# Optimization experiments

Hardware: AMD Instinct MI355X
Metric: run time of the kernel (lower is better)

## Reference

```python
import jax, jax.numpy as jnp
import numpy as np

# lct_fk config (matches init_kwargs)
BIN_LEN = 0.01
WALL_SIZE = 2.0
C_LIGHT = 3.0e8


def _safe_sqrt(v):
    # sqrt(relu(v)) with a well-defined (zero) subgradient at v<=0
    pos = v > 0
    return jnp.where(pos, jnp.sqrt(jnp.where(pos, v, 1.0)), 0.0)


def _trilinear_zero(vol, pz, py, px):
    # vol: (D,H,W) complex64; pz/py/px: (D2,H2,W2) float pixel coords
    # Trilinear sampling with zeros padding (== F.grid_sample align_corners=False)
    D, H, W = vol.shape
    z0f = jnp.floor(pz); y0f = jnp.floor(py); x0f = jnp.floor(px)
    dz = pz - z0f; dy = py - y0f; dx = px - x0f
    z0 = z0f.astype(jnp.int32); y0 = y0f.astype(jnp.int32); x0 = x0f.astype(jnp.int32)
    out = jnp.zeros(pz.shape, vol.dtype)
    for iz, wz in ((z0, 1.0 - dz), (z0 + 1, dz)):
        for iy, wy in ((y0, 1.0 - dy), (y0 + 1, dy)):
            for ix, wx in ((x0, 1.0 - dx), (x0 + 1, dx)):
                valid = (iz >= 0) & (iz < D) & (iy >= 0) & (iy < H) & (ix >= 0) & (ix < W)
                v = vol[jnp.clip(iz, 0, D - 1), jnp.clip(iy, 0, H - 1), jnp.clip(ix, 0, W - 1)]
                w = jnp.where(valid, wz * wy * wx, 0.0)
                out = out + w * v
    return out


def setup_inputs() -> dict:
    key = jax.random.key(0)
    feture = jax.random.uniform(key, (1, 2, 128, 128, 128), dtype=jnp.float32)
    return {"feture_bxdxtxhxw": feture}


def reference(feture_bxdxtxhxw):
    b, d, T, H, W = feture_bxdxtxhxw.shape
    M, N = T, H  # temprol_grid (== crop), sptial_grid; tbes=0, tens=crop -> no temporal pad
    width = WALL_SIZE / 2.0
    trange = M * BIN_LEN  # crop * c * (bin_len/c)

    # z-weighting: (z/(M-1))^2, then sqrt(relu(.))
    gridz = (jnp.arange(M, dtype=jnp.float32) / (M - 1)).reshape(1, M, 1, 1)
    data = feture_bxdxtxhxw.reshape(b * d, T, H, W) * (gridz ** 2)
    data = _safe_sqrt(jax.nn.relu(data))

    # zero-pad to (2T,2H,2W), FFT, fftshift (roll by half == fftshift for even sizes)
    datapad = jnp.pad(data, ((0, 0), (0, M), (0, N), (0, N)))
    fre = jnp.fft.fftshift(jnp.fft.fftn(datapad, axes=(-3, -2, -1)), axes=(-3, -2, -1))

    # Stolt (f-k) warped coordinates, normalized to [-1,1]
    zdim = (jnp.arange(2 * M, dtype=jnp.float32) - M) / M
    xdim = (jnp.arange(2 * N, dtype=jnp.float32) - N) / N
    gz = zdim[:, None, None]            # varies along axis 0
    gy = xdim[None, :, None]            # varies along axis 1
    gx = xdim[None, None, :]            # varies along axis 2
    fk = (N * trange / (M * width * 4.0)) ** 2
    gznew = jnp.sqrt(fk * (gx ** 2 + gy ** 2) + gz ** 2)  # (2M,2N,2N)
    gznew = jnp.broadcast_to(gznew, (2 * M, 2 * N, 2 * N))

    # unnormalize (align_corners=False): pix = ((c+1)*size - 1)/2
    px = ((jnp.broadcast_to(gx, gznew.shape) + 1.0) * (2 * N) - 1.0) * 0.5
    py = ((jnp.broadcast_to(gy, gznew.shape) + 1.0) * (2 * N) - 1.0) * 0.5
    pz = ((gznew + 1.0) * (2 * M) - 1.0) * 0.5

    samp = jax.vmap(lambda v: _trilinear_zero(v, pz, py, px))(fre)

    # zero negative/zero frequencies along z, then Stolt Jacobian scaling
    z0pos = M + 1  # first index where zdim > 0
    zmask = (jnp.arange(2 * M) >= z0pos)[None, :, None, None]
    samp = samp * zmask
    samp = samp * (jnp.abs(gz) / (gznew + 1e-8))[None]

    samp = jnp.fft.fftshift(samp, axes=(-3, -2, -1))  # ifftshift == fftshift (even dims)
    vol = jnp.fft.ifftn(samp, axes=(-3, -2, -1))
    out = vol[:, :M, :N, :N].real
    return out.reshape(b, d, M, N, N)
```

## Files before the change

### kernel.cpp

```cpp
#include <hip/hip_runtime.h>

static constexpr size_t VS   = 8388608;
static constexpr int    ZSTR = 65536;
static constexpr int    YSTR = 256;
static constexpr size_t VSB  = 4194304;
static constexpr int    BZS  = 32768;
static constexpr int    BYS  = 128;
static constexpr int    LSTR = 261;

typedef float vf2 __attribute__((ext_vector_type(2)));
typedef _Float16 h2 __attribute__((ext_vector_type(2)));

__device__ __forceinline__ unsigned pkh(vf2 a){
    h2 h; h.x = (_Float16)a.x; h.y = (_Float16)a.y;
    return __builtin_bit_cast(unsigned, h);
}
__device__ __forceinline__ vf2 uph(unsigned u){
    h2 h = __builtin_bit_cast(h2, u);
    vf2 r; r.x = (float)h.x; r.y = (float)h.y; return r;
}

__device__ __forceinline__ vf2 cmul(vf2 a, vf2 b){
    vf2 asw; asw.x = -a.y; asw.y = a.x;
    return a*b.x + asw*b.y;
}

constexpr int BREV(int k){ return ((k&1)<<3)|((k&2)<<1)|((k&4)>>1)|((k&8)>>3); }

__device__ __forceinline__ void bf(vf2& a, vf2& b, float c, float s){
    vf2 sum = a + b;
    vf2 dif = a - b;
    vf2 dsw; dsw.x = -dif.y; dsw.y = dif.x;
    b = dif*c + dsw*s;
    a = sum;
}

template<int DIR>
__device__ __forceinline__ void fft16(vf2 r[16]){
    constexpr float D = (float)DIR;
    constexpr float C16[8] = {1.f, 0.92387953f, 0.70710678f, 0.38268343f, 0.f, -0.38268343f, -0.70710678f, -0.92387953f};
    constexpr float S16[8] = {0.f, 0.38268343f, 0.70710678f, 0.92387953f, 1.f, 0.92387953f, 0.70710678f, 0.38268343f};
#pragma unroll
    for (int j = 0; j < 8; ++j) bf(r[j], r[j+8], C16[j], D*S16[j]);
    constexpr float C8[4] = {1.f, 0.70710678f, 0.f, -0.70710678f};
    constexpr float S8[4] = {0.f, 0.70710678f, 1.f, 0.70710678f};
#pragma unroll
    for (int g = 0; g < 16; g += 8)
#pragma unroll
        for (int j = 0; j < 4; ++j) bf(r[g+j], r[g+j+4], C8[j], D*S8[j]);
#pragma unroll
    for (int g = 0; g < 16; g += 4){
        bf(r[g],   r[g+2], 1.f, 0.f);
        bf(r[g+1], r[g+3], 0.f, D);
    }
#pragma unroll
    for (int g = 0; g < 16; g += 2) bf(r[g], r[g+1], 1.f, 0.f);
}

__device__ __forceinline__ void init_tw(vf2* tw, float dir){
    int tid = threadIdx.x;
    float ang = dir * 0.0245436926f * (float)((tid >> 4)*(tid & 15));
    float s, c; __sincosf(ang, &s, &c);
    vf2 w; w.x = c; w.y = s;
    tw[tid] = w;
}

template<int DIR>
__device__ __forceinline__ void mid256t2(vf2 r[2][16], unsigned* shp, const vf2* tw, int t, int l){
#pragma unroll
    for (int c = 0; c < 2; ++c) fft16<DIR>(r[c]);
#pragma unroll
    for (int k1 = 1; k1 < 16; ++k1){
        vf2 w = tw[k1*16 + t];
        r[0][BREV(k1)] = cmul(r[0][BREV(k1)], w);
        r[1][BREV(k1)] = cmul(r[1][BREV(k1)], w);
    }
    int lr = l & 7;
    bool lo = (l < 8);
    if (lo){
#pragma unroll
        for (int c = 0; c < 2; ++c)
#pragma unroll
            for (int k1 = 0; k1 < 16; ++k1)
                shp[(lr*2 + c)*LSTR + k1*16 + (t ^ k1)] = pkh(r[c][BREV(k1)]);
    }
    __syncthreads();
    if (lo){
#pragma unroll
        for (int c = 0; c < 2; ++c)
#pragma unroll
            for (int n2 = 0; n2 < 16; ++n2)
                r[c][n2] = uph(shp[(lr*2 + c)*LSTR + t*16 + (n2 ^ t)]);
    }
    __syncthreads();
    if (!lo){
#pragma unroll
        for (int c = 0; c < 2; ++c)
#pragma unroll
            for (int k1 = 0; k1 < 16; ++k1)
                shp[(lr*2 + c)*LSTR + k1*16 + (t ^ k1)] = pkh(r[c][BREV(k1)]);
    }
    __syncthreads();
    if (!lo){
#pragma unroll
        for (int c = 0; c < 2; ++c)
#pragma unroll
            for (int n2 = 0; n2 < 16; ++n2)
                r[c][n2] = uph(shp[(lr*2 + c)*LSTR + t*16 + (n2 ^ t)]);
    }
#pragma unroll
    for (int c = 0; c < 2; ++c) fft16<DIR>(r[c]);
}

template<int DIR>
__device__ __forceinline__ void twiddle_reg(vf2 r[16], int t){
    float sn, cn; __sincosf((float)DIR * 0.0245436926f * (float)t, &sn, &cn);
    vf2 w; w.x = cn; w.y = sn;
    vf2 wk = w;
#pragma unroll
    for (int k1 = 1; k1 < 16; ++k1){
        r[BREV(k1)] = cmul(r[BREV(k1)], wk);
        wk = cmul(wk, w);
    }
}

__device__ __forceinline__ void wave_transpose(vf2 r[16], vf2* shw, int t, int l){
    vf2* base = shw + ((l >> 2)*2 + (l & 1))*LSTR;
    if ((l & 2) == 0){
#pragma unroll
        for (int k1 = 0; k1 < 16; ++k1) base[k1*16 + (t ^ k1)] = r[BREV(k1)];
#pragma unroll
        for (int n2 = 0; n2 < 16; ++n2) r[n2] = base[t*16 + (n2 ^ t)];
    }
    __builtin_amdgcn_sched_barrier(0);
    if ((l & 2) != 0){
#pragma unroll
        for (int k1 = 15; k1 >= 0; --k1) base[k1*16 + (t ^ k1)] = r[BREV(k1)];
#pragma unroll
        for (int n2 = 15; n2 >= 0; --n2) r[n2] = base[t*16 + (n2 ^ t)];
    }
}

template<int DIR>
__device__ __forceinline__ void mid256wr(vf2 r[16], vf2* shw, int t, int l){
    fft16<DIR>(r);
    twiddle_reg<DIR>(r, t);
    wave_transpose(r, shw, t, l);
    fft16<DIR>(r);
}

template<int DIR, int NIN, int NOUT>
__device__ __forceinline__ void fft_strided2(unsigned* g, int S, float insc){
    __shared__ unsigned shp[16*LSTR];
    __shared__ vf2 tw[256];
    int t = threadIdx.x >> 4, l = threadIdx.x & 15;
    vf2 r[2][16];
    vf2 zero; zero.x = 0.f; zero.y = 0.f;
#pragma unroll
    for (int n1 = 0; n1 < 16; ++n1){
        if (n1 < NIN/16){
            uint2 ld = *reinterpret_cast<const uint2*>(&g[(size_t)(16*n1 + t)*S + 2*l]);
            r[0][n1] = uph(ld.x)*insc;
            r[1][n1] = uph(ld.y)*insc;
        } else { r[0][n1] = zero; r[1][n1] = zero; }
    }
    init_tw(tw, (float)DIR);
    __syncthreads();
    mid256t2<DIR>(r, shp, tw, t, l);
#pragma unroll
    for (int k2 = 0; k2 < 16; ++k2)
        if (k2 < NOUT/16){
            uint2 st; st.x = pkh(r[0][BREV(k2)]); st.y = pkh(r[1][BREV(k2)]);
            *reinterpret_cast<uint2*>(&g[(size_t)(t + 16*k2)*S + 2*l]) = st;
        }
}

__global__ void __launch_bounds__(256) k_p1(const float* __restrict__ in, unsigned* __restrict__ A){
    __shared__ vf2 sh8[8*LSTR];
    int tid = threadIdx.x, bid = blockIdx.x;
    int yc = bid & 7, z = (bid >> 3) & 127, v = bid >> 10;
    int t = tid & 15, l = tid >> 4;
    float gz = z * (1.0f/127.0f);
    float g2 = gz*gz;
    const float* src = in + (((size_t)(v*128 + z))*128 + yc*16 + l)*128;
    float val[8];
#pragma unroll
    for (int n1 = 0; n1 < 8; ++n1) val[n1] = src[16*n1 + t];
#pragma unroll
    for (int n1 = 0; n1 < 8; ++n1){
        float x = val[n1] * g2;
        val[n1] = x > 0.f ? sqrtf(x) : 0.f;
    }
    float part = ((val[0]+val[1]) + (val[2]+val[3])) + ((val[4]+val[5]) + (val[6]+val[7]));
    part = (t & 1) ? -part : part;
    part += __shfl_xor(part, 1);
    part += __shfl_xor(part, 2);
    part += __shfl_xor(part, 4);
    part += __shfl_xor(part, 8);
    vf2 r[16];
    vf2 zero; zero.x = 0.f; zero.y = 0.f;
#pragma unroll
    for (int n1 = 8; n1 < 16; ++n1) r[n1] = zero;
#pragma unroll
    for (int n1 = 0; n1 < 8; ++n1){
        float sn, cn; __sincosf(0.0245436926f * (float)(16*n1 + t), &sn, &cn);
        r[n1].x = val[n1] * 0.5f * (1.f + cn);
        r[n1].y = val[n1] * 0.5f * sn;
    }
    mid256wr<-1>(r, sh8, t, l);
    if (t == 0){ r[1].x = part*0.5f; r[1].y = 0.f; }
    unsigned* dst = A + (size_t)v*VS + (size_t)z*ZSTR + (size_t)(yc*16 + l)*YSTR;
#pragma unroll
    for (int k2 = 0; k2 < 16; ++k2)
        dst[t + 16*k2] = pkh(r[BREV(k2)]);
}

__global__ void __launch_bounds__(256) k_p2z(unsigned* __restrict__ A){
    int bid = blockIdx.x;
    int xb = bid & 7, y = (bid >> 3) & 127, v = bid >> 10;
    fft_strided2<-1,128,128>(A + (size_t)v*VS + (size_t)y*YSTR + xb*32, ZSTR, 1.f);
}

__global__ void __launch_bounds__(256) k_p3y(unsigned* __restrict__ A){
    __shared__ unsigned shp[16*LSTR];
    __shared__ vf2 tw[256];
    __shared__ vf2 shW[128];
    const float SC3 = 0.015625f;
    int bid = blockIdx.x;
    int xb = bid & 7, z = (bid >> 3) & 127, v = bid >> 10;
    unsigned* g = A + (size_t)v*VS + (size_t)z*ZSTR + xb*32;
    int t = threadIdx.x >> 4, l = threadIdx.x & 15;
    vf2 r[2][16];
    vf2 zero; zero.x = 0.f; zero.y = 0.f;
#pragma unroll
    for (int n1 = 0; n1 < 16; ++n1){
        if (n1 < 8){
            uint2 ld = *reinterpret_cast<const uint2*>(&g[(size_t)(16*n1 + t)*YSTR + 2*l]);
            r[0][n1] = uph(ld.x);
            r[1][n1] = uph(ld.y);
        } else { r[0][n1] = zero; r[1][n1] = zero; }
    }
#pragma unroll
    for (int c = 0; c < 2; ++c){
        vf2 part = ((r[c][0]+r[c][1]) + (r[c][2]+r[c][3])) + ((r[c][4]+r[c][5]) + (r[c][6]+r[c][7]));
        part = part * ((t & 1) ? -1.f : 1.f);
        part.x += __shfl_xor(part.x, 16);
        part.y += __shfl_xor(part.y, 16);
        part.x += __shfl_xor(part.x, 32);
        part.y += __shfl_xor(part.y, 32);
        if ((t & 3) == 0) shW[(t >> 2)*32 + 2*l + c] = part;
    }
#pragma unroll
    for (int n1 = 0; n1 < 8; ++n1){
        float sn, cn; __sincosf(0.0245436926f * (float)(16*n1 + t), &sn, &cn);
        vf2 c; c.x = SC3*0.5f*(1.f + cn); c.y = SC3*0.5f*sn;
        r[0][n1] = cmul(r[0][n1], c);
        r[1][n1] = cmul(r[1][n1], c);
    }
    init_tw(tw, -1.f);
    __syncthreads();
    mid256t2<-1>(r, shp, tw, t, l);
    if (t == 0){
#pragma unroll
        for (int c = 0; c < 2; ++c){
            vf2 S = (shW[2*l + c] + shW[32 + 2*l + c]) + (shW[64 + 2*l + c] + shW[96 + 2*l + c]);
            r[c][BREV(8)] = S * (0.5f*SC3);
        }
    }
#pragma unroll
    for (int k2 = 0; k2 < 16; ++k2){
        uint2 st; st.x = pkh(r[0][BREV(k2)]); st.y = pkh(r[1][BREV(k2)]);
        *reinterpret_cast<uint2*>(&g[(size_t)(t + 16*k2)*YSTR + 2*l]) = st;
    }
}

__global__ void __launch_bounds__(256) k_p45(const unsigned* __restrict__ A, unsigned* __restrict__ B){
    __shared__ vf2 sh8[8*LSTR];
    int tid = threadIdx.x, bid = blockIdx.x;
    int yc = bid & 15, zn = (bid >> 4) & 127, v = bid >> 11;
    const unsigned* Av = A + (size_t)v*VS;
    int t = tid & 15, l = tid >> 4;
    int yn = yc*16 + l;
    float gy = (yn < 128 ? yn : yn - 256) * (1.0f/128.0f);
    float gz = zn * (1.0f/128.0f);
    float c2 = 0.1024f*gy*gy + gz*gz;
    unsigned rowoff = (unsigned)yn*YSTR;
    vf2 r[16];
#pragma unroll
    for (int n1 = 0; n1 < 16; ++n1){
        int xn = 16*n1 + t;
        float gx = (xn < 128 ? xn : xn - 256) * (1.0f/128.0f);
        float s2 = c2 + 0.1024f*gx*gx;
        float rs = __builtin_amdgcn_rsqf(s2 + 1e-12f);
        float gznew = s2 * rs;
        float pz = gznew*128.0f + 127.5f;
        int zi = (int)pz;
        float dz = pz - (float)zi;
        int zp0 = zi - 128;
        float wf = gz * rs;
        float w0 = (((unsigned)zp0     < 128u) ? (1.0f - dz) : 0.f) * wf;
        float w1 = (((unsigned)(zp0+1) < 128u) ? dz : 0.f) * wf;
        vf2 v0 = uph(Av[(size_t)((unsigned)(zp0 & 127) * ZSTR) + rowoff + xn]);
        vf2 v1 = uph(Av[(size_t)((unsigned)((zp0 + 1) & 127) * ZSTR) + rowoff + xn]);
        r[n1] = v0*w0 + v1*w1;
    }
    mid256wr<1>(r, sh8, t, l);
    unsigned* dst = B + (size_t)v*VSB + (size_t)zn*BZS + (size_t)yn*BYS;
#pragma unroll
    for (int k2 = 0; k2 < 8; ++k2)
        dst[t + 16*k2] = pkh(r[BREV(k2)]);
}

__global__ void __launch_bounds__(256) k_p6(unsigned* __restrict__ B){
    int bid = blockIdx.x;
    int xb = bid & 3, zn = (bid >> 2) & 127, v = bid >> 9;
    fft_strided2<1,256,128>(B + (size_t)v*VSB + (size_t)zn*BZS + xb*32, BYS, 0.00390625f);
}

__global__ void __launch_bounds__(256) k_p7(const unsigned* __restrict__ B, float* __restrict__ out){
    __shared__ unsigned shp[16*LSTR];
    __shared__ vf2 tw[256];
    const float sc = 9.765625e-4f;
    int bid = blockIdx.x;
    int xb = bid & 3, y = (bid >> 2) & 127, v = bid >> 9;
    const unsigned* g = B + (size_t)v*VSB + (size_t)y*BYS + xb*32;
    int t = threadIdx.x >> 4, l = threadIdx.x & 15;
    vf2 r[2][16];
    vf2 zero; zero.x = 0.f; zero.y = 0.f;
#pragma unroll
    for (int n1 = 0; n1 < 16; ++n1){
        if (n1 < 8){
            uint2 ld = *reinterpret_cast<const uint2*>(&g[(size_t)(16*n1 + t)*BZS + 2*l]);
            r[0][n1] = uph(ld.x)*sc;
            r[1][n1] = uph(ld.y)*sc;
        } else { r[0][n1] = zero; r[1][n1] = zero; }
    }
    init_tw(tw, 1.f);
    __syncthreads();
    mid256t2<1>(r, shp, tw, t, l);
    float* dst = out + ((size_t)(v*128)*128 + y)*128 + xb*32 + 2*l;
#pragma unroll
    for (int k2 = 0; k2 < 8; ++k2){
        float2 st; st.x = r[0][BREV(k2)].x; st.y = r[1][BREV(k2)].x;
        *reinterpret_cast<float2*>(&dst[(size_t)(t + 16*k2)*16384]) = st;
    }
}

extern "C" void kernel_launch(void* const* d_in, const int* in_sizes, int n_in,
                              void* d_out, int out_size, void* d_ws, size_t ws_size,
                              hipStream_t stream){
    const float* in = (const float*)d_in[0];
    float* out = (float*)d_out;
    unsigned* A = (unsigned*)d_ws;
    unsigned* B = A + 2*VS;
    k_p1 <<< 2048, 256, 0, stream>>>(in, A);
    k_p2z<<< 2048, 256, 0, stream>>>(A);
    k_p3y<<< 2048, 256, 0, stream>>>(A);
    k_p45<<< 4096, 256, 0, stream>>>(A, B);
    k_p6 <<< 1024, 256, 0, stream>>>(B);
    k_p7 <<< 1024, 256, 0, stream>>>(B, out);
}
```

Baseline: 184.1 us.

## Fuse x-FFT and z-FFT passes into one kernel over shared-memory xz planes

Merges the first pass (preprocess plus x-axis FFT) and the z-axis FFT into a single kernel. Each 512-thread block holds a whole 128x256 xz plane for one y in LDS, runs the x FFTs per row, then the z FFTs per column, and writes the plane out once with coalesced 16-byte stores. This removes one full global write and read of the half-precision spectrum, plus a launch. In exchange it uses a large LDS footprint and only 256 blocks, so occupancy and load balance across CUs may suffer.

```diff
diff --git a/kernel.cpp b/kernel.cpp
--- a/kernel.cpp
+++ b/kernel.cpp
@@ -7,6 +7,7 @@
 static constexpr int    BZS  = 32768;
 static constexpr int    BYS  = 128;
 static constexpr int    LSTR = 261;
+static constexpr int    PSTR = 260;
 
 typedef float vf2 __attribute__((ext_vector_type(2)));
 typedef _Float16 h2 __attribute__((ext_vector_type(2)));
@@ -62,7 +63,7 @@
     float ang = dir * 0.0245436926f * (float)((tid >> 4)*(tid & 15));
     float s, c; __sincosf(ang, &s, &c);
     vf2 w; w.x = c; w.y = s;
-    tw[tid] = w;
+    if (tid < 256) tw[tid] = w;
 }
 
 template<int DIR>
@@ -175,50 +176,117 @@
         }
 }
 
-__global__ void __launch_bounds__(256) k_p1(const float* __restrict__ in, unsigned* __restrict__ A){
-    __shared__ vf2 sh8[8*LSTR];
+__global__ void __launch_bounds__(512) k_p1xz(const float* __restrict__ in, unsigned* __restrict__ A){
+    __shared__ unsigned plane[128*PSTR];
+    __shared__ unsigned shp[16*LSTR];
+    __shared__ vf2 tw[256];
     int tid = threadIdx.x, bid = blockIdx.x;
-    int yc = bid & 7, z = (bid >> 3) & 127, v = bid >> 10;
-    int t = tid & 15, l = tid >> 4;
-    float gz = z * (1.0f/127.0f);
-    float g2 = gz*gz;
-    const float* src = in + (((size_t)(v*128 + z))*128 + yc*16 + l)*128;
-    float val[8];
-#pragma unroll
-    for (int n1 = 0; n1 < 8; ++n1) val[n1] = src[16*n1 + t];
-#pragma unroll
-    for (int n1 = 0; n1 < 8; ++n1){
-        float x = val[n1] * g2;
-        val[n1] = x > 0.f ? sqrtf(x) : 0.f;
-    }
-    float part = ((val[0]+val[1]) + (val[2]+val[3])) + ((val[4]+val[5]) + (val[6]+val[7]));
-    part = (t & 1) ? -part : part;
-    part += __shfl_xor(part, 1);
-    part += __shfl_xor(part, 2);
-    part += __shfl_xor(part, 4);
-    part += __shfl_xor(part, 8);
-    vf2 r[16];
-    vf2 zero; zero.x = 0.f; zero.y = 0.f;
-#pragma unroll
-    for (int n1 = 8; n1 < 16; ++n1) r[n1] = zero;
+    int y = bid & 127, v = bid >> 7;
+    init_tw(tw, -1.f);
+    int t = tid & 15, g = tid >> 4;
+
+    float valr[4][8];
+#pragma unroll
+    for (int rr = 0; rr < 4; ++rr){
+        int z = g + 32*rr;
+        const float* src = in + (size_t)(v*128 + z)*16384 + (size_t)y*128;
+#pragma unroll
+        for (int n1 = 0; n1 < 8; ++n1) valr[rr][n1] = src[16*n1 + t];
+    }
+    vf2 cp[8];
 #pragma unroll
     for (int n1 = 0; n1 < 8; ++n1){
         float sn, cn; __sincosf(0.0245436926f * (float)(16*n1 + t), &sn, &cn);
-        r[n1].x = val[n1] * 0.5f * (1.f + cn);
-        r[n1].y = val[n1] * 0.5f * sn;
-    }
-    mid256wr<-1>(r, sh8, t, l);
-    if (t == 0){ r[1].x = part*0.5f; r[1].y = 0.f; }
-    unsigned* dst = A + (size_t)v*VS + (size_t)z*ZSTR + (size_t)(yc*16 + l)*YSTR;
-#pragma unroll
-    for (int k2 = 0; k2 < 16; ++k2)
-        dst[t + 16*k2] = pkh(r[BREV(k2)]);
-}
-
-__global__ void __launch_bounds__(256) k_p2z(unsigned* __restrict__ A){
-    int bid = blockIdx.x;
-    int xb = bid & 7, y = (bid >> 3) & 127, v = bid >> 10;
-    fft_strided2<-1,128,128>(A + (size_t)v*VS + (size_t)y*YSTR + xb*32, ZSTR, 1.f);
+        cp[n1].x = 0.5f*(1.f + cn); cp[n1].y = 0.5f*sn;
+    }
+#pragma unroll
+    for (int rr = 0; rr < 4; ++rr){
+        int z = g + 32*rr;
+        float gz = z * (1.0f/127.0f);
+        float g2 = gz*gz;
+        float val[8];
+#pragma unroll
+        for (int n1 = 0; n1 < 8; ++n1){
+            float xv = valr[rr][n1] * g2;
+            val[n1] = xv > 0.f ? sqrtf(xv) : 0.f;
+        }
+        float part = ((val[0]+val[1])+(val[2]+val[3]))+((val[4]+val[5])+(val[6]+val[7]));
+        part = (t & 1) ? -part : part;
+        part += __shfl_xor(part, 1);
+        part += __shfl_xor(part, 2);
+        part += __shfl_xor(part, 4);
+        part += __shfl_xor(part, 8);
+        vf2 r[16];
+        vf2 zero; zero.x = 0.f; zero.y = 0.f;
+#pragma unroll
+        for (int n1 = 8; n1 < 16; ++n1) r[n1] = zero;
+#pragma unroll
+        for (int n1 = 0; n1 < 8; ++n1){ r[n1].x = val[n1]*cp[n1].x; r[n1].y = val[n1]*cp[n1].y; }
+        fft16<-1>(r);
+        twiddle_reg<-1>(r, t);
+        unsigned* pr = plane + z*PSTR;
+#pragma unroll
+        for (int k1 = 0; k1 < 16; ++k1) pr[k1*16 + (t ^ k1)] = pkh(r[BREV(k1)]);
+#pragma unroll
+        for (int n2 = 0; n2 < 16; ++n2) r[n2] = uph(pr[t*16 + (n2 ^ t)]);
+        fft16<-1>(r);
+        if (t == 0){ r[1].x = part*0.5f; r[1].y = 0.f; }
+#pragma unroll
+        for (int k2 = 0; k2 < 16; ++k2) pr[t + 16*k2] = pkh(r[BREV(k2)]);
+    }
+    __syncthreads();
+
+    unsigned colin[8][8];
+#pragma unroll
+    for (int cc = 0; cc < 8; ++cc){
+        int x = g + 32*cc;
+#pragma unroll
+        for (int n1 = 0; n1 < 8; ++n1)
+            colin[cc][n1] = plane[(16*n1 + t)*PSTR + x];
+    }
+    __syncthreads();
+#pragma unroll
+    for (int cc = 0; cc < 8; ++cc){
+        int x = g + 32*cc;
+        vf2 r[16];
+        vf2 zero; zero.x = 0.f; zero.y = 0.f;
+#pragma unroll
+        for (int n1 = 0; n1 < 8; ++n1) r[n1] = uph(colin[cc][n1]);
+#pragma unroll
+        for (int n1 = 8; n1 < 16; ++n1) r[n1] = zero;
+        fft16<-1>(r);
+#pragma unroll
+        for (int k1 = 1; k1 < 16; ++k1)
+            r[BREV(k1)] = cmul(r[BREV(k1)], tw[k1*16 + t]);
+        unsigned* sb = shp + ((g >> 2)*2 + (g & 1))*LSTR;
+        if ((g & 2) == 0){
+#pragma unroll
+            for (int k1 = 0; k1 < 16; ++k1) sb[k1*16 + (t ^ k1)] = pkh(r[BREV(k1)]);
+#pragma unroll
+            for (int n2 = 0; n2 < 16; ++n2) r[n2] = uph(sb[t*16 + (n2 ^ t)]);
+        }
+        __builtin_amdgcn_sched_barrier(0);
+        if ((g & 2) != 0){
+#pragma unroll
+            for (int k1 = 15; k1 >= 0; --k1) sb[k1*16 + (t ^ k1)] = pkh(r[BREV(k1)]);
+#pragma unroll
+            for (int n2 = 15; n2 >= 0; --n2) r[n2] = uph(sb[t*16 + (n2 ^ t)]);
+        }
+        fft16<-1>(r);
+#pragma unroll
+        for (int k2 = 0; k2 < 8; ++k2)
+            plane[(t + 16*k2)*PSTR + x] = pkh(r[BREV(k2)]);
+    }
+    __syncthreads();
+
+    unsigned* dstA = A + (size_t)v*VS + (size_t)y*YSTR;
+#pragma unroll
+    for (int i = 0; i < 16; ++i){
+        int linear = (tid + 512*i)*4;
+        int z = linear >> 8, x = linear & 255;
+        uint4 val = *reinterpret_cast<const uint4*>(&plane[z*PSTR + x]);
+        *reinterpret_cast<uint4*>(&dstA[(size_t)z*ZSTR + x]) = val;
+    }
 }
 
 __global__ void __launch_bounds__(256) k_p3y(unsigned* __restrict__ A){
@@ -353,10 +421,9 @@
     float* out = (float*)d_out;
     unsigned* A = (unsigned*)d_ws;
     unsigned* B = A + 2*VS;
-    k_p1 <<< 2048, 256, 0, stream>>>(in, A);
-    k_p2z<<< 2048, 256, 0, stream>>>(A);
-    k_p3y<<< 2048, 256, 0, stream>>>(A);
-    k_p45<<< 4096, 256, 0, stream>>>(A, B);
-    k_p6 <<< 1024, 256, 0, stream>>>(B);
-    k_p7 <<< 1024, 256, 0, stream>>>(B, out);
-}
+    k_p1xz<<<  256, 512, 0, stream>>>(in, A);
+    k_p3y <<< 2048, 256, 0, stream>>>(A);
+    k_p45 <<< 4096, 256, 0, stream>>>(A, B);
+    k_p6  <<< 1024, 256, 0, stream>>>(B);
+    k_p7  <<< 1024, 256, 0, stream>>>(B, out);
+}
```

After: 188.0 us. 1.02x slower.
